# Kernel optimization log

Hardware: AMD Instinct MI355X
Metric: run time of the kernel (lower is better)

The kernel has to match this reference:

```python
import jax, jax.numpy as jnp
import numpy as np


def setup_inputs() -> dict:
    key = jax.random.key(0)
    k1, k2, k3 = jax.random.split(key, 3)
    B, V, C = 2, 20000, 9
    KS, OUT, NB = 9, 16, 16
    x = jax.random.normal(k1, (B, V, C), dtype=jnp.float32)
    # Glorot-normal-ish init for W [coord, kernel_size, out]
    W = jax.random.normal(k2, (C, KS, OUT), dtype=jnp.float32) * np.sqrt(2.0 / (C + KS * OUT)).astype(np.float32)
    # adj indexes a zero-padded vertex table of size V+1; 0 means 'no neighbor'
    adj = jax.random.randint(k3, (V, NB), 0, V + 1, dtype=jnp.int32)
    return {"x": x, "W": W, "adj": adj}


def reference(x, W, adj):
    B, V, C = x.shape
    _, KS, OUT = W.shape  # note: code only runs when C == KS (source bug, see notes)
    NB = adj.shape[1]
    # degree normalization: 1/count_nonzero(adj) per vertex, 0 if no neighbors
    deg = jnp.sum(adj != 0, axis=-1).astype(x.dtype)  # [V]
    inv_deg = jnp.where(deg > 0, 1.0 / jnp.where(deg > 0, deg, 1.0), 0.0)  # [V]
    # wx = x @ reshape(W, [C, KS*OUT])
    wx = jnp.einsum('bvc,cf->bvf', x, W.reshape(C, KS * OUT))  # [B,V,KS*OUT]
    zero_pad = jnp.zeros((B, 1, KS * OUT), dtype=x.dtype)
    patches = jnp.concatenate([zero_pad, wx], axis=1)[:, adj]  # [B,V,NB,KS*OUT]
    patches = patches.reshape(B, V, NB, KS, OUT)
    # pseudo-coordinate diffs on padded raw input
    pad_x = jnp.concatenate([jnp.zeros((B, 1, C), dtype=x.dtype), x], axis=1)
    nbx = pad_x[:, adj]  # [B,V,NB,C]
    mask = (adj != 0)[None, :, :, None]
    diff = jnp.where(mask, x[:, :, None, :] - nbx, jnp.zeros_like(nbx))  # [B,V,NB,C]
    # source bug: matmul with u is discarded; softmax over coord axis
    q = jax.nn.softmax(diff, axis=-1)  # [B,V,NB,C] with C == KS
    # weighted aggregation over neighbors, then degree norm, then sum over kernels
    agg = jnp.einsum('bvnk,bvnko->bvko', q, patches)  # [B,V,KS,OUT]
    agg = agg * inv_deg[None, :, None, None]
    out = jnp.sum(agg, axis=2)  # [B,V,OUT]
    return jax.nn.relu(out)
```

## Files before the change

### kernel.cpp

```cpp
#include <hip/hip_runtime.h>
#include <math.h>

#define Bb   2
#define Vv   20000
#define Cc   9
#define KS   9
#define OUTn 16
#define NB   16

__global__ __launch_bounds__(256) void nlayer_kernel(
    const float* __restrict__ x,
    const float* __restrict__ W,
    const int*   __restrict__ adj,
    float* __restrict__ out)
{
    __shared__ float sW[Cc * KS * OUTn];
    for (int i = threadIdx.x; i < Cc * KS * OUTn; i += 256) sW[i] = W[i];
    __syncthreads();

    int tid = blockIdx.x * 256 + threadIdx.x;
    if (tid >= Bb * Vv) return;
    int b = tid / Vv;
    int v = tid - b * Vv;

    int a[NB];
    #pragma unroll
    for (int n = 0; n < NB; ++n) a[n] = adj[v * NB + n];

    int deg = 0;
    #pragma unroll
    for (int n = 0; n < NB; ++n) deg += (a[n] != 0);

    const float* xb = x + (size_t)b * Vv * Cc;

    float xv[Cc];
    #pragma unroll
    for (int c = 0; c < Cc; ++c) xv[c] = xb[(size_t)v * Cc + c];

    float s[KS][Cc];
    #pragma unroll
    for (int k = 0; k < KS; ++k)
        #pragma unroll
        for (int c = 0; c < Cc; ++c) s[k][c] = 0.0f;

    for (int n = 0; n < NB; ++n) {
        int j = a[n];
        if (j == 0) continue;
        const float* xp = xb + (size_t)(j - 1) * Cc;
        float xn[Cc];
        #pragma unroll
        for (int c = 0; c < Cc; ++c) xn[c] = xp[c];

        float d[Cc];
        float m = -INFINITY;
        #pragma unroll
        for (int c = 0; c < Cc; ++c) { d[c] = xv[c] - xn[c]; m = fmaxf(m, d[c]); }
        float e[Cc];
        float sum = 0.0f;
        #pragma unroll
        for (int c = 0; c < Cc; ++c) { e[c] = __expf(d[c] - m); sum += e[c]; }
        float inv = 1.0f / sum;

        #pragma unroll
        for (int k = 0; k < KS; ++k) {
            float qk = e[k] * inv;
            #pragma unroll
            for (int c = 0; c < Cc; ++c) s[k][c] = fmaf(qk, xn[c], s[k][c]);
        }
    }

    float invdeg = (deg > 0) ? (1.0f / (float)deg) : 0.0f;

    float acc[OUTn];
    #pragma unroll
    for (int o = 0; o < OUTn; ++o) acc[o] = 0.0f;

    #pragma unroll
    for (int c = 0; c < Cc; ++c) {
        #pragma unroll
        for (int k = 0; k < KS; ++k) {
            float sv = s[k][c];
            const float* wp = &sW[(c * KS + k) * OUTn];
            #pragma unroll
            for (int o = 0; o < OUTn; ++o) acc[o] = fmaf(sv, wp[o], acc[o]);
        }
    }

    float* op = out + (size_t)tid * OUTn;
    #pragma unroll
    for (int o = 0; o < OUTn; ++o) {
        float r = acc[o] * invdeg;
        op[o] = (r > 0.0f) ? r : 0.0f;
    }
}

extern "C" void kernel_launch(void* const* d_in, const int* in_sizes, int n_in,
                              void* d_out, int out_size, void* d_ws, size_t ws_size,
                              hipStream_t stream) {
    const float* x   = (const float*)d_in[0];
    const float* W   = (const float*)d_in[1];
    const int*   adj = (const int*)d_in[2];
    float*       out = (float*)d_out;

    const int total = Bb * Vv;
    const int block = 256;
    const int grid  = (total + block - 1) / block;
    nlayer_kernel<<<grid, block, 0, stream>>>(x, W, adj, out);
}
```

Baseline: 72.46 us.

## Split each vertex across four threads and gather from padded 16B-aligned copy

```diff
diff --git a/kernel.cpp b/kernel.cpp
--- a/kernel.cpp
+++ b/kernel.cpp
@@ -7,9 +7,32 @@
 #define KS   9
 #define OUTn 16
 #define NB   16
+#define PADC 12
+
+__global__ __launch_bounds__(256) void prepad_kernel(
+    const float* __restrict__ x, float* __restrict__ xpad)
+{
+    int t = blockIdx.x * 256 + threadIdx.x;
+    if (t >= Bb * (Vv + 1)) return;
+    int b = t / (Vv + 1);
+    int j = t - b * (Vv + 1);
+
+    float r[PADC];
+    #pragma unroll
+    for (int c = 0; c < PADC; ++c) r[c] = 0.0f;
+    if (j > 0) {
+        const float* src = x + ((size_t)b * Vv + (j - 1)) * Cc;
+        #pragma unroll
+        for (int c = 0; c < Cc; ++c) r[c] = src[c];
+    }
+    float4* dst = (float4*)(xpad + (size_t)t * PADC);
+    dst[0] = make_float4(r[0], r[1], r[2],  r[3]);
+    dst[1] = make_float4(r[4], r[5], r[6],  r[7]);
+    dst[2] = make_float4(r[8], r[9], r[10], r[11]);
+}
 
 __global__ __launch_bounds__(256) void nlayer_kernel(
-    const float* __restrict__ x,
+    const float* __restrict__ xpad,
     const float* __restrict__ W,
     const int*   __restrict__ adj,
     float* __restrict__ out)
@@ -18,24 +41,26 @@
     for (int i = threadIdx.x; i < Cc * KS * OUTn; i += 256) sW[i] = W[i];
     __syncthreads();
 
-    int tid = blockIdx.x * 256 + threadIdx.x;
-    if (tid >= Bb * Vv) return;
-    int b = tid / Vv;
-    int v = tid - b * Vv;
+    int t    = blockIdx.x * 256 + threadIdx.x;
+    int pair = t >> 2;
+    int sub  = t & 3;
+    if (pair >= Bb * Vv) return;
+    int b = pair / Vv;
+    int v = pair - b * Vv;
 
-    int a[NB];
-    #pragma unroll
-    for (int n = 0; n < NB; ++n) a[n] = adj[v * NB + n];
+    const float* xb = xpad + (size_t)b * (Vv + 1) * PADC;
+
+    const float4* xvp = (const float4*)(xb + (size_t)(v + 1) * PADC);
+    float4 xv0 = xvp[0], xv1 = xvp[1];
+    float  xv8 = ((const float*)&xvp[2])[0];
+    float xv[Cc] = {xv0.x, xv0.y, xv0.z, xv0.w, xv1.x, xv1.y, xv1.z, xv1.w, xv8};
+
+    int4 av = *(const int4*)(adj + (size_t)v * NB + (sub << 2));
+    int a[4] = {av.x, av.y, av.z, av.w};
 
     int deg = 0;
     #pragma unroll
-    for (int n = 0; n < NB; ++n) deg += (a[n] != 0);
-
-    const float* xb = x + (size_t)b * Vv * Cc;
-
-    float xv[Cc];
-    #pragma unroll
-    for (int c = 0; c < Cc; ++c) xv[c] = xb[(size_t)v * Cc + c];
+    for (int i = 0; i < 4; ++i) deg += (a[i] != 0);
 
     float s[KS][Cc];
     #pragma unroll
@@ -43,13 +68,13 @@
         #pragma unroll
         for (int c = 0; c < Cc; ++c) s[k][c] = 0.0f;
 
-    for (int n = 0; n < NB; ++n) {
-        int j = a[n];
-        if (j == 0) continue;
-        const float* xp = xb + (size_t)(j - 1) * Cc;
-        float xn[Cc];
-        #pragma unroll
-        for (int c = 0; c < Cc; ++c) xn[c] = xp[c];
+    #pragma unroll
+    for (int i = 0; i < 4; ++i) {
+        int j = a[i];
+        const float4* np = (const float4*)(xb + (size_t)j * PADC);
+        float4 n0 = np[0], n1 = np[1];
+        float  n8 = ((const float*)&np[2])[0];
+        float xn[Cc] = {n0.x, n0.y, n0.z, n0.w, n1.x, n1.y, n1.z, n1.w, n8};
 
         float d[Cc];
         float m = -INFINITY;
@@ -69,29 +94,40 @@
         }
     }
 
+    #pragma unroll
+    for (int k = 0; k < KS; ++k) {
+        #pragma unroll
+        for (int c = 0; c < Cc; ++c) {
+            float vv = s[k][c];
+            vv += __shfl_xor(vv, 1);
+            vv += __shfl_xor(vv, 2);
+            s[k][c] = vv;
+        }
+    }
+    deg += __shfl_xor(deg, 1);
+    deg += __shfl_xor(deg, 2);
     float invdeg = (deg > 0) ? (1.0f / (float)deg) : 0.0f;
 
-    float acc[OUTn];
-    #pragma unroll
-    for (int o = 0; o < OUTn; ++o) acc[o] = 0.0f;
-
+    float acc0 = 0.f, acc1 = 0.f, acc2 = 0.f, acc3 = 0.f;
     #pragma unroll
     for (int c = 0; c < Cc; ++c) {
         #pragma unroll
         for (int k = 0; k < KS; ++k) {
             float sv = s[k][c];
-            const float* wp = &sW[(c * KS + k) * OUTn];
-            #pragma unroll
-            for (int o = 0; o < OUTn; ++o) acc[o] = fmaf(sv, wp[o], acc[o]);
+            float4 w = *(const float4*)&sW[(c * KS + k) * OUTn + (sub << 2)];
+            acc0 = fmaf(sv, w.x, acc0);
+            acc1 = fmaf(sv, w.y, acc1);
+            acc2 = fmaf(sv, w.z, acc2);
+            acc3 = fmaf(sv, w.w, acc3);
         }
     }
 
-    float* op = out + (size_t)tid * OUTn;
-    #pragma unroll
-    for (int o = 0; o < OUTn; ++o) {
-        float r = acc[o] * invdeg;
-        op[o] = (r > 0.0f) ? r : 0.0f;
-    }
+    float4 r;
+    r.x = fmaxf(acc0 * invdeg, 0.0f);
+    r.y = fmaxf(acc1 * invdeg, 0.0f);
+    r.z = fmaxf(acc2 * invdeg, 0.0f);
+    r.w = fmaxf(acc3 * invdeg, 0.0f);
+    *(float4*)(out + (size_t)pair * OUTn + (sub << 2)) = r;
 }
 
 extern "C" void kernel_launch(void* const* d_in, const int* in_sizes, int n_in,
@@ -101,9 +137,14 @@
     const float* W   = (const float*)d_in[1];
     const int*   adj = (const int*)d_in[2];
     float*       out = (float*)d_out;
+    float*       xpad = (float*)d_ws;
 
-    const int total = Bb * Vv;
-    const int block = 256;
-    const int grid  = (total + block - 1) / block;
-    nlayer_kernel<<<grid, block, 0, stream>>>(x, W, adj, out);
+    {
+        int total = Bb * (Vv + 1);
+        prepad_kernel<<<(total + 255) / 256, 256, 0, stream>>>(x, xpad);
+    }
+    {
+        int total = Bb * Vv * 4;
+        nlayer_kernel<<<(total + 255) / 256, 256, 0, stream>>>(xpad, W, adj, out);
+    }
 }
```

After: 78.89 us. +8.9%, slower.
